# Optimization experiments

Hardware: AMD Instinct MI355X
Metric: run time of the kernel (lower is better)

## Reference

```python
import jax, jax.numpy as jnp
import numpy as np

N_HEAD = 8
HIDDEN = 512
EPS_LN = 1e-3  # keras LayerNormalization default epsilon


def layernorm(x, gamma, beta, eps=EPS_LN):
    mu = jnp.mean(x, axis=-1, keepdims=True)
    var = jnp.mean((x - mu) ** 2, axis=-1, keepdims=True)
    return (x - mu) * jax.lax.rsqrt(var + eps) * gamma + beta


def setup_inputs() -> dict:
    key = jax.random.key(0)
    ks = jax.random.split(key, 10)
    bs, NE, F = 512, 128, HIDDEN
    x = jax.random.normal(ks[0], (bs, NE, F), dtype=jnp.float32)
    mask = (jax.random.uniform(ks[1], (bs, 1, NE)) < 0.85).astype(jnp.float32)
    # guarantee at least one live entity per row
    mask = mask.at[:, :, 0].set(1.0)
    s = 1.0 / np.sqrt(F)
    Wqk = jax.random.normal(ks[2], (F, 2 * HIDDEN), dtype=jnp.float32) * s
    bqk = jnp.zeros((2 * HIDDEN,), jnp.float32)
    Wv = jax.random.normal(ks[3], (F, HIDDEN), dtype=jnp.float32) * s
    bv = jnp.zeros((HIDDEN,), jnp.float32)
    Wmlp = jax.random.normal(ks[4], (F, HIDDEN), dtype=jnp.float32) * s
    bmlp = jnp.zeros((HIDDEN,), jnp.float32)
    g_pre = jnp.ones((F,), jnp.float32)
    b_pre = jnp.zeros((F,), jnp.float32)
    g_post = jnp.ones((F,), jnp.float32)
    b_post = jnp.zeros((F,), jnp.float32)
    return dict(x=x, mask=mask, Wqk=Wqk, bqk=bqk, Wv=Wv, bv=bv,
                Wmlp=Wmlp, bmlp=bmlp, g_pre=g_pre, b_pre=b_pre,
                g_post=g_post, b_post=b_post)


def reference(x, mask, Wqk, bqk, Wv, bv, Wmlp, bmlp, g_pre, b_pre, g_post, b_post):
    bs, NE, F = x.shape
    h, d = N_HEAD, HIDDEN // N_HEAD
    x4 = x[:, None]  # (bs, 1, NE, F)

    # pre-norm only feeds qkv projections; residual uses raw x4
    inp = layernorm(x4, g_pre, b_pre)

    qk = (inp @ Wqk + bqk).reshape(bs, 1, NE, h, d, 2)
    q, k = qk[..., 0], qk[..., 1]                       # (bs,1,NE,h,d)
    v = (inp @ Wv + bv).reshape(bs, 1, NE, h, d)

    logits = jnp.einsum('btnhd,btmhd->bthnm', q, k) / np.sqrt(d)  # (bs,1,h,NE,NE)

    m5 = mask[:, :, None, None, :]                      # (bs,1,1,1,NE)
    logits = logits - (1.0 - m5) * 1e10
    logits = logits - jnp.max(logits, axis=-1, keepdims=True)
    un = jnp.exp(logits) * m5
    p = un / (jnp.sum(un, axis=-1, keepdims=True) + 1e-10)
    p = p * m5

    att = jnp.einsum('bthnm,btmhd->btnhd', p, v).reshape(bs, 1, NE, HIDDEN)
    a = att @ Wmlp + bmlp                               # mlp_layer=1, no activation
    y = x4 + a                                          # residual
    y = layernorm(y, g_post, b_post)

    # masked average pooling over entities
    mE = mask[..., None]                                # (bs,1,NE,1)
    pooled = jnp.sum(y * mE, axis=-2) / (jnp.sum(mE, axis=-2) + 1e-5)  # (bs,1,F)
    return pooled.reshape(bs, F)
```

## Files before the change

kernel.cpp:

```cpp
#include <hip/hip_runtime.h>
#include <hip/hip_bf16.h>


typedef __bf16 bf16;
typedef __bf16 bf16x8 __attribute__((ext_vector_type(8)));
typedef __bf16 bf16x4 __attribute__((ext_vector_type(4)));
typedef float f32x4 __attribute__((ext_vector_type(4)));
typedef unsigned u32x4 __attribute__((ext_vector_type(4)));

__device__ __forceinline__ f32x4 mfma16(bf16x8 a, bf16x8 b, f32x4 c) {
    return __builtin_amdgcn_mfma_f32_16x16x32_bf16(a, b, c, 0, 0, 0);
}

typedef const unsigned int __attribute__((address_space(1)))* gptr_t;
typedef unsigned int __attribute__((address_space(3)))* lptr_t;
__device__ __forceinline__ void gld16(const void* g, void* l) {
    __builtin_amdgcn_global_load_lds((gptr_t)g, (lptr_t)l, 16, 0, 0);
}

__device__ __forceinline__ unsigned pack2(float lo, float hi) {
    unsigned short a = __builtin_bit_cast(unsigned short, (bf16)lo);
    unsigned short b = __builtin_bit_cast(unsigned short, (bf16)hi);
    return (unsigned)a | ((unsigned)b << 16);
}

#define SWZ(byteoff, row) ((byteoff) ^ (((row) & 7) << 4))


__global__ __launch_bounds__(256) void prep_split_kernel(
    const float* __restrict__ Wqk, const float* __restrict__ bqk,
    const float* __restrict__ Wv, const float* __restrict__ bv,
    const float* __restrict__ Wmlp,
    bf16* __restrict__ Wqkv_s, bf16* __restrict__ Wmlp_t, float* __restrict__ bQKV)
{
    int t = blockIdx.x * 256 + threadIdx.x;
    if (t < 524288) {
        int k = t >> 10, c = t & 1023;
        int h = c >> 7, w7 = c & 127, d = w7 >> 1, isK = w7 & 1;
        int n = isK * 512 + h * 64 + d;
        int tn = n >> 7, nc = n & 127, kc = k >> 6, kw = k & 63;
        Wqkv_s[((size_t)(tn * 8 + kc) * 128 + nc) * 64 + kw] = (bf16)Wqk[t];
    } else if (t < 786432) {
        int u = t - 524288;
        int k = u >> 9, c = u & 511;
        int n = 1024 + c;
        int tn = n >> 7, nc = n & 127, kc = k >> 6, kw = k & 63;
        Wqkv_s[((size_t)(tn * 8 + kc) * 128 + nc) * 64 + kw] = (bf16)Wv[u];
    } else if (t < 1048576) {
        int u = t - 786432;
        int k = u >> 9, c = u & 511;
        int tn = c >> 7, nc = c & 127, kc = k >> 6, kw = k & 63;
        Wmlp_t[((size_t)(tn * 8 + kc) * 128 + nc) * 64 + kw] = (bf16)Wmlp[u];
    } else if (t < 1050112) {
        int j = t - 1048576;
        int region = j >> 9, w9 = j & 511, h = w9 >> 6, d = w9 & 63;
        float v;
        if (region == 0)      v = bqk[h * 128 + d * 2];
        else if (region == 1) v = bqk[h * 128 + d * 2 + 1];
        else                  v = bv[h * 64 + d];
        bQKV[j] = v;
    }
}

__global__ __launch_bounds__(256) void ln_kernel(
    const float* __restrict__ x, const float* __restrict__ g,
    const float* __restrict__ b, bf16* __restrict__ inp)
{
    int row = blockIdx.x * 4 + (threadIdx.x >> 6);
    int lane = threadIdx.x & 63;
    int k0 = lane * 8;
    const float* xr = x + (size_t)row * 512 + k0;
    f32x4 a0 = *(const f32x4*)xr;
    f32x4 a1 = *(const f32x4*)(xr + 4);
    float s = 0.f, ss = 0.f;
#pragma unroll
    for (int i = 0; i < 4; i++) {
        s += a0[i] + a1[i];
        ss += a0[i] * a0[i] + a1[i] * a1[i];
    }
#pragma unroll
    for (int m = 1; m < 64; m <<= 1) {
        s  += __shfl_xor(s, m, 64);
        ss += __shfl_xor(ss, m, 64);
    }
    float mu = s * (1.f / 512.f);
    float rstd = rsqrtf(ss * (1.f / 512.f) - mu * mu + 1e-3f);
    f32x4 g0 = *(const f32x4*)(g + k0);
    f32x4 g1 = *(const f32x4*)(g + k0 + 4);
    f32x4 b0 = *(const f32x4*)(b + k0);
    f32x4 b1 = *(const f32x4*)(b + k0 + 4);
    bf16x8 ov;
#pragma unroll
    for (int i = 0; i < 4; i++) {
        ov[i]     = (bf16)((a0[i] - mu) * rstd * g0[i] + b0[i]);
        ov[i + 4] = (bf16)((a1[i] - mu) * rstd * g1[i] + b1[i]);
    }
    *(bf16x8*)(inp + (size_t)row * 512 + k0) = ov;
}

__global__ __launch_bounds__(256) void qkv_gemm_kernel(
    const bf16* __restrict__ inp, const bf16* __restrict__ Wqkv_s,
    const float* __restrict__ bQKV,
    bf16* __restrict__ q, bf16* __restrict__ kbuf, bf16* __restrict__ vt)
{
    __shared__ __align__(16) bf16 As[128 * 64];
    __shared__ __align__(16) bf16 Bs[128 * 64];
    const int bid = blockIdx.x;
    const int idx = (bid & 7) * 768 + (bid >> 3);
    const int tm = idx / 12, tn = idx % 12;
    const int tid = threadIdx.x;
    const int w = tid >> 6, l = tid & 63;
    const int wr = w >> 1, wc = w & 1;
    const int l15 = l & 15, l4 = l >> 4;

    const f32x4 fz = {0.f, 0.f, 0.f, 0.f};
    f32x4 acc[4][4];
#pragma unroll
    for (int m = 0; m < 4; m++)
#pragma unroll
        for (int n = 0; n < 4; n++) acc[m][n] = fz;

    const int arow = l >> 3;
    const int axc = ((l & 7) ^ arow) * 8;
    const bf16* Abase = inp + (size_t)(tm * 128) * 512;
    const int rsw = (l15 & 7) << 4;

    for (int kc = 0; kc < 8; kc++) {
#pragma unroll
        for (int i = 0; i < 4; i++) {
            int rg = (i * 4 + w) * 8;
            gld16(Abase + (size_t)(rg + arow) * 512 + kc * 64 + axc,
                  As + (i * 4 + w) * 512);
        }
        const bf16* Bbase = Wqkv_s + (size_t)(tn * 8 + kc) * 8192;
#pragma unroll
        for (int i = 0; i < 4; i++) {
            gld16(Bbase + (size_t)((i * 4 + w) * 8 + arow) * 64 + axc,
                  Bs + (i * 4 + w) * 512);
        }
        __syncthreads();
#pragma unroll
        for (int kk = 0; kk < 2; kk++) {
            const int kb = (kk * 64 + l4 * 16) ^ rsw;
            bf16x8 af[4], bfr[4];
#pragma unroll
            for (int m = 0; m < 4; m++)
                af[m] = *(const bf16x8*)((const char*)As + (wr * 64 + m * 16 + l15) * 128 + kb);
#pragma unroll
            for (int n = 0; n < 4; n++)
                bfr[n] = *(const bf16x8*)((const char*)Bs + (wc * 64 + n * 16 + l15) * 128 + kb);
#pragma unroll
            for (int m = 0; m < 4; m++)
#pragma unroll
                for (int n = 0; n < 4; n++)
                    acc[m][n] = mfma16(af[m], bfr[n], acc[m][n]);
        }
        __syncthreads();
    }

    const int colBase = tn * 128 + wc * 64;
    const int mrowBase = tm * 128 + wr * 64;
#pragma unroll
    for (int n = 0; n < 4; n++) {
        int col = colBase + n * 16 + l15;
        float bias = bQKV[col];
        int within = col & 511, hh = within >> 6, dd = within & 63;
#pragma unroll
        for (int m = 0; m < 4; m++) {
            int mr0 = mrowBase + m * 16 + l4 * 4;
            int bb = mr0 >> 7, e0 = mr0 & 127;
            size_t base = (size_t)(bb * 8 + hh) * 8192;
            if (tn < 4) {
#pragma unroll
                for (int r = 0; r < 4; r++)
                    q[base + (size_t)(e0 + r) * 64 + dd] = (bf16)(acc[m][n][r] + bias);
            } else if (tn < 8) {
#pragma unroll
                for (int r = 0; r < 4; r++) {
                    int e = e0 + r;
                    kbuf[base + (size_t)e * 64 + (dd ^ ((e & 7) << 3))] = (bf16)(acc[m][n][r] + bias);
                }
            } else {
                bf16x4 pk;
#pragma unroll
                for (int r = 0; r < 4; r++) pk[r] = (bf16)(acc[m][n][r] + bias);
                *(bf16x4*)(vt + base + (size_t)dd * 128 + (e0 ^ ((dd & 7) << 3))) = pk;
            }
        }
    }
}

__global__ __launch_bounds__(512) void attn_fused_kernel(
    const bf16* __restrict__ q, const bf16* __restrict__ kbuf,
    const bf16* __restrict__ vt, const float* __restrict__ mask,
    bf16* __restrict__ att)
{
    __shared__ __align__(16) char Ks[2][128 * 128];
    __shared__ __align__(16) char VTs[2][64 * 256];
    __shared__ float mrow[128];

    const int b = blockIdx.x;
    const size_t bh0 = (size_t)b * 8;
    const int tid = threadIdx.x;
    const int w = tid >> 6, l = tid & 63;
    const int l15 = l & 15, l4 = l >> 4, R0 = w * 16;

    if (tid < 128) mrow[tid] = mask[b * 128 + tid];

    {
        const bf16* kb = kbuf + bh0 * 8192;
        const bf16* vb = vt + bh0 * 8192;
#pragma unroll
        for (int i = 0; i < 2; i++) {
            gld16(kb + ((i * 8 + w) * 64 + l) * 8, (bf16*)Ks[0] + (i * 8 + w) * 512);
            gld16(vb + ((i * 8 + w) * 64 + l) * 8, (bf16*)VTs[0] + (i * 8 + w) * 512);
        }
    }
    const bf16* qp0 = q + bh0 * 8192 + (size_t)(R0 + l15) * 64 + l4 * 8;
    bf16x8 afn0 = *(const bf16x8*)(qp0);
    bf16x8 afn1 = *(const bf16x8*)(qp0 + 32);
    __syncthreads();

    const f32x4 fz = {0.f, 0.f, 0.f, 0.f};
    for (int h = 0; h < 8; h++) {
        const int cur = h & 1;
        bf16x8 af0 = afn0, af1 = afn1;
        if (h < 7) {
            const bf16* kb = kbuf + (bh0 + h + 1) * 8192;
            const bf16* vb = vt + (bh0 + h + 1) * 8192;
#pragma unroll
            for (int i = 0; i < 2; i++) {
                gld16(kb + ((i * 8 + w) * 64 + l) * 8, (bf16*)Ks[cur ^ 1] + (i * 8 + w) * 512);
                gld16(vb + ((i * 8 + w) * 64 + l) * 8, (bf16*)VTs[cur ^ 1] + (i * 8 + w) * 512);
            }
            const bf16* qp = q + (bh0 + h + 1) * 8192 + (size_t)(R0 + l15) * 64 + l4 * 8;
            afn0 = *(const bf16x8*)(qp);
            afn1 = *(const bf16x8*)(qp + 32);
        }

        f32x4 accL[8];
#pragma unroll
        for (int n = 0; n < 8; n++) accL[n] = fz;
#pragma unroll
        for (int ks = 0; ks < 2; ks++) {
            bf16x8 bq = ks ? af1 : af0;
            const int k2 = ks * 64 + l4 * 16;
#pragma unroll
            for (int nt = 0; nt < 8; nt++) {
                const int krow = nt * 16 + l15;
                bf16x8 kf = *(const bf16x8*)(Ks[cur] + krow * 128 + (k2 ^ ((krow & 7) << 4)));
                accL[nt] = mfma16(kf, bq, accL[nt]);
            }
        }

        float mx = -1e30f;
#pragma unroll
        for (int nt = 0; nt < 8; nt++)
#pragma unroll
            for (int r = 0; r < 4; r++) {
                float mk = mrow[nt * 16 + l4 * 4 + r];
                float v = accL[nt][r] * 0.125f - (1.0f - mk) * 1e10f;
                accL[nt][r] = v;
                mx = fmaxf(mx, v);
            }
        mx = fmaxf(mx, __shfl_xor(mx, 16, 64));
        mx = fmaxf(mx, __shfl_xor(mx, 32, 64));
        float sum = 0.f;
#pragma unroll
        for (int nt = 0; nt < 8; nt++)
#pragma unroll
            for (int r = 0; r < 4; r++) {
                float mk = mrow[nt * 16 + l4 * 4 + r];
                float e = __expf(accL[nt][r] - mx) * mk;
                accL[nt][r] = e;
                sum += e;
            }
        sum += __shfl_xor(sum, 16, 64);
        sum += __shfl_xor(sum, 32, 64);
        const float inv = 1.0f / (sum + 1e-10f);

        unsigned pk[8][2];
#pragma unroll
        for (int nt = 0; nt < 8; nt++)
#pragma unroll
            for (int qq = 0; qq < 2; qq++)
                pk[nt][qq] = pack2(accL[nt][2 * qq] * inv, accL[nt][2 * qq + 1] * inv);

        f32x4 accO[4];
#pragma unroll
        for (int n = 0; n < 4; n++) accO[n] = fz;
        const int glo = l15 + ((l4 & 1) << 5);
#pragma unroll
        for (int ks = 0; ks < 4; ks++) {
            u32x4 pa4;
#pragma unroll
            for (int p = 0; p < 4; p++) {
                int srcl = glo + ((p >> 1) << 4);
                unsigned va = (unsigned)__shfl((int)pk[2 * ks][p & 1], srcl, 64);
                unsigned vb = (unsigned)__shfl((int)pk[2 * ks + 1][p & 1], srcl, 64);
                pa4[p] = (l4 & 2) ? vb : va;
            }
            bf16x8 pa = __builtin_bit_cast(bf16x8, pa4);
            const int e2 = ks * 64 + l4 * 16;
#pragma unroll
            for (int nt = 0; nt < 4; nt++) {
                const int d = nt * 16 + l15;
                bf16x8 vf = *(const bf16x8*)(VTs[cur] + d * 256 + (e2 ^ ((d & 7) << 4)));
                accO[nt] = mfma16(pa, vf, accO[nt]);
            }
        }

        bf16* outp = att + (size_t)(b * 128) * 512 + h * 64;
#pragma unroll
        for (int nt = 0; nt < 4; nt++) {
            const int d = nt * 16 + l15;
#pragma unroll
            for (int r = 0; r < 4; r++) {
                const int e = R0 + l4 * 4 + r;
                outp[(size_t)e * 512 + d] = (bf16)accO[nt][r];
            }
        }
        __syncthreads();
    }
}

__global__ __launch_bounds__(256) void mlp_gemm_kernel(
    const bf16* __restrict__ att, const bf16* __restrict__ Wmlp_t,
    const float* __restrict__ bmlp, float* __restrict__ y)
{
    __shared__ __align__(16) bf16 As[128 * 64];
    __shared__ __align__(16) bf16 Bs[128 * 64];
    const int bid = blockIdx.x;
    const int idx = (bid & 7) * 256 + (bid >> 3);
    const int tm = idx >> 2, tn = idx & 3;
    const int tid = threadIdx.x;
    const int w = tid >> 6, l = tid & 63;
    const int wr = w >> 1, wc = w & 1;
    const int l15 = l & 15, l4 = l >> 4;

    const f32x4 fz = {0.f, 0.f, 0.f, 0.f};
    f32x4 acc[4][4];
#pragma unroll
    for (int m = 0; m < 4; m++)
#pragma unroll
        for (int n = 0; n < 4; n++) acc[m][n] = fz;

    const int arow = l >> 3;
    const int axc = ((l & 7) ^ arow) * 8;
    const bf16* Abase = att + (size_t)(tm * 128) * 512;
    const int rsw = (l15 & 7) << 4;

    for (int kc = 0; kc < 8; kc++) {
#pragma unroll
        for (int i = 0; i < 4; i++) {
            int rg = (i * 4 + w) * 8;
            gld16(Abase + (size_t)(rg + arow) * 512 + kc * 64 + axc,
                  As + (i * 4 + w) * 512);
        }
        const bf16* Bbase = Wmlp_t + (size_t)(tn * 8 + kc) * 8192;
#pragma unroll
        for (int i = 0; i < 4; i++) {
            gld16(Bbase + (size_t)((i * 4 + w) * 8 + arow) * 64 + axc,
                  Bs + (i * 4 + w) * 512);
        }
        __syncthreads();
#pragma unroll
        for (int kk = 0; kk < 2; kk++) {
            const int kb = (kk * 64 + l4 * 16) ^ rsw;
            bf16x8 af[4], bfr[4];
#pragma unroll
            for (int m = 0; m < 4; m++)
                af[m] = *(const bf16x8*)((const char*)As + (wr * 64 + m * 16 + l15) * 128 + kb);
#pragma unroll
            for (int n = 0; n < 4; n++)
                bfr[n] = *(const bf16x8*)((const char*)Bs + (wc * 64 + n * 16 + l15) * 128 + kb);
#pragma unroll
            for (int m = 0; m < 4; m++)
#pragma unroll
                for (int n = 0; n < 4; n++)
                    acc[m][n] = mfma16(af[m], bfr[n], acc[m][n]);
        }
        __syncthreads();
    }

    const int colBase = tn * 128 + wc * 64;
    const int mrowBase = tm * 128 + wr * 64;
#pragma unroll
    for (int n = 0; n < 4; n++) {
        int col = colBase + n * 16 + l15;
        float bias = bmlp[col];
#pragma unroll
        for (int m = 0; m < 4; m++) {
            int row0 = mrowBase + m * 16 + l4 * 4;
#pragma unroll
            for (int r = 0; r < 4; r++)
                y[(size_t)(row0 + r) * 512 + col] = acc[m][n][r] + bias;
        }
    }
}

__global__ __launch_bounds__(512) void pool_kernel(
    const float* __restrict__ y, const float* __restrict__ x,
    const float* __restrict__ mask, const float* __restrict__ gpost,
    const float* __restrict__ bpost, float* __restrict__ out)
{
    __shared__ float partial[8][512];
    __shared__ float mrow[128];
    __shared__ float msum_s;

    const int b = blockIdx.x;
    const int tid = threadIdx.x;
    const int w = tid >> 6, l = tid & 63;
    const int k0 = l * 8;

    if (tid < 128) mrow[tid] = mask[b * 128 + tid];
    __syncthreads();
    if (w == 0) {
        float v = mrow[l] + mrow[64 + l];
#pragma unroll
        for (int m = 1; m < 64; m <<= 1) v += __shfl_xor(v, m, 64);
        if (l == 0) msum_s = v;
    }

    f32x4 g0 = *(const f32x4*)(gpost + k0);
    f32x4 g1 = *(const f32x4*)(gpost + k0 + 4);
    f32x4 b0 = *(const f32x4*)(bpost + k0);
    f32x4 b1 = *(const f32x4*)(bpost + k0 + 4);

    f32x4 a0 = {0.f, 0.f, 0.f, 0.f}, a1 = {0.f, 0.f, 0.f, 0.f};
    for (int i = 0; i < 16; i++) {
        int row = w * 16 + i;
        const float* yr = y + ((size_t)(b * 128 + row)) * 512 + k0;
        const float* xr = x + ((size_t)(b * 128 + row)) * 512 + k0;
        f32x4 v0 = *(const f32x4*)yr + *(const f32x4*)xr;
        f32x4 v1 = *(const f32x4*)(yr + 4) + *(const f32x4*)(xr + 4);
        float s = 0.f, ss = 0.f;
#pragma unroll
        for (int j = 0; j < 4; j++) {
            s += v0[j] + v1[j];
            ss += v0[j] * v0[j] + v1[j] * v1[j];
        }
#pragma unroll
        for (int m = 1; m < 64; m <<= 1) {
            s  += __shfl_xor(s, m, 64);
            ss += __shfl_xor(ss, m, 64);
        }
        float mu = s * (1.f / 512.f);
        float rstd = rsqrtf(ss * (1.f / 512.f) - mu * mu + 1e-3f);
        float mr = mrow[row];
#pragma unroll
        for (int j = 0; j < 4; j++) {
            a0[j] += ((v0[j] - mu) * rstd * g0[j] + b0[j]) * mr;
            a1[j] += ((v1[j] - mu) * rstd * g1[j] + b1[j]) * mr;
        }
    }
#pragma unroll
    for (int j = 0; j < 4; j++) {
        partial[w][k0 + j]     = a0[j];
        partial[w][k0 + 4 + j] = a1[j];
    }
    __syncthreads();
    float t = 0.f;
#pragma unroll
    for (int ww = 0; ww < 8; ww++) t += partial[ww][tid];
    out[(size_t)b * 512 + tid] = t / (msum_s + 1e-5f);
}

__global__ __launch_bounds__(256) void prep_kernel(
    const float* __restrict__ Wqk, const float* __restrict__ bqk,
    const float* __restrict__ Wv, const float* __restrict__ bv,
    const float* __restrict__ Wmlp,
    bf16* __restrict__ Wqkv_t, bf16* __restrict__ Wmlp_t, float* __restrict__ bQKV)
{
    int t = blockIdx.x * 256 + threadIdx.x;
    const int NQKV = 8 * 192 * 512;
    if (t < NQKV) {
        int h = t / (192 * 512);
        int rem = t - h * (192 * 512);
        int n = rem >> 9;
        int k = rem & 511;
        float v;
        if (n < 64)       v = Wqk[k * 1024 + h * 128 + n * 2];
        else if (n < 128) v = Wqk[k * 1024 + h * 128 + (n - 64) * 2 + 1];
        else              v = Wv[k * 512 + h * 64 + (n - 128)];
        Wqkv_t[t] = (bf16)v;
    } else {
        int u = t - NQKV;
        if (u < 512 * 512) {
            int col = u >> 9, k = u & 511;
            Wmlp_t[u] = (bf16)Wmlp[k * 512 + col];
        } else {
            int j = u - 512 * 512;
            if (j < 1536) {
                int h = j / 192, n = j - h * 192;
                float v;
                if (n < 64)       v = bqk[h * 128 + n * 2];
                else if (n < 128) v = bqk[h * 128 + (n - 64) * 2 + 1];
                else              v = bv[h * 64 + (n - 128)];
                bQKV[j] = v;
            }
        }
    }
}

__global__ __launch_bounds__(512) void attn_kernel(
    const bf16* __restrict__ inp, const float* __restrict__ mask,
    const bf16* __restrict__ Wqkv_t, const float* __restrict__ bQKV,
    bf16* __restrict__ att)
{
    __shared__ __align__(16) char Qs[128 * 128];
    __shared__ __align__(16) char Ks[128 * 128];
    __shared__ __align__(16) char VTs[64 * 256];
    __shared__ __align__(16) char Ps[128 * 256];
    __shared__ float mrow[128];

    const int bid = blockIdx.x;
    const int b = bid & 511;
    const int h = bid >> 9;
    const int tid = threadIdx.x;
    const int w = tid >> 6, l = tid & 63;
    const int l15 = l & 15, l4 = l >> 4;
    const int R0 = w * 16;

    if (tid < 128) mrow[tid] = mask[b * 128 + tid];

    const bf16* A  = inp + (size_t)(b * 128) * 512;
    const bf16* Wh = Wqkv_t + (size_t)h * 192 * 512;
    const f32x4 fz = {0.f, 0.f, 0.f, 0.f};

    f32x4 acc[12];
#pragma unroll
    for (int n = 0; n < 12; n++) acc[n] = fz;
    const bf16* aptr = A + (size_t)(R0 + l15) * 512 + l4 * 8;
#pragma unroll 4
    for (int ks = 0; ks < 16; ks++) {
        bf16x8 af = *(const bf16x8*)(aptr + ks * 32);
#pragma unroll
        for (int n = 0; n < 12; n++) {
            bf16x8 bfr = *(const bf16x8*)(Wh + (size_t)(n * 16 + l15) * 512 + ks * 32 + l4 * 8);
            acc[n] = mfma16(af, bfr, acc[n]);
        }
    }
#pragma unroll
    for (int n = 0; n < 12; n++) {
        int col = n * 16 + l15;
        float bias = bQKV[h * 192 + col];
#pragma unroll
        for (int r = 0; r < 4; r++) {
            int row = R0 + l4 * 4 + r;
            bf16 val = (bf16)(acc[n][r] + bias);
            if (n < 4) {
                *(bf16*)(Qs + row * 128 + SWZ(col * 2, row)) = val;
            } else if (n < 8) {
                *(bf16*)(Ks + row * 128 + SWZ((col - 64) * 2, row)) = val;
            } else {
                int d = col - 128;
                *(bf16*)(VTs + d * 256 + SWZ(row * 2, d)) = val;
            }
        }
    }
    __syncthreads();

    f32x4 accL[8];
#pragma unroll
    for (int n = 0; n < 8; n++) accL[n] = fz;
#pragma unroll
    for (int ks = 0; ks < 2; ks++) {
        int k = ks * 32 + l4 * 8;
        int qrow = R0 + l15;
        bf16x8 af = *(const bf16x8*)(Qs + qrow * 128 + SWZ(k * 2, qrow));
#pragma unroll
        for (int nt = 0; nt < 8; nt++) {
            int krow = nt * 16 + l15;
            bf16x8 bfr = *(const bf16x8*)(Ks + krow * 128 + SWZ(k * 2, krow));
            accL[nt] = mfma16(af, bfr, accL[nt]);
        }
    }
    float pv[32];
#pragma unroll
    for (int r = 0; r < 4; r++) {
        float mx = -1e30f;
#pragma unroll
        for (int nt = 0; nt < 8; nt++) {
            int colk = nt * 16 + l15;
            float v = accL[nt][r] * 0.125f - (1.0f - mrow[colk]) * 1e10f;
            pv[nt * 4 + r] = v;
            mx = fmaxf(mx, v);
        }
#pragma unroll
        for (int m = 1; m < 16; m <<= 1) mx = fmaxf(mx, __shfl_xor(mx, m, 64));
        float sum = 0.f;
#pragma unroll
        for (int nt = 0; nt < 8; nt++) {
            int colk = nt * 16 + l15;
            float e = __expf(pv[nt * 4 + r] - mx) * mrow[colk];
            pv[nt * 4 + r] = e;
            sum += e;
        }
#pragma unroll
        for (int m = 1; m < 16; m <<= 1) sum += __shfl_xor(sum, m, 64);
        float inv = 1.0f / (sum + 1e-10f);
        int prow = R0 + l4 * 4 + r;
#pragma unroll
        for (int nt = 0; nt < 8; nt++) {
            bf16 pb = (bf16)(pv[nt * 4 + r] * inv);
            *(bf16*)(Ps + prow * 256 + SWZ((nt * 16 + l15) * 2, prow)) = pb;
        }
    }
    __syncthreads();

    f32x4 accO[4];
#pragma unroll
    for (int n = 0; n < 4; n++) accO[n] = fz;
#pragma unroll
    for (int ks = 0; ks < 4; ks++) {
        int k = ks * 32 + l4 * 8;
        int prow = R0 + l15;
        bf16x8 af = *(const bf16x8*)(Ps + prow * 256 + SWZ(k * 2, prow));
#pragma unroll
        for (int nt = 0; nt < 4; nt++) {
            int d = nt * 16 + l15;
            bf16x8 bfr = *(const bf16x8*)(VTs + d * 256 + SWZ(k * 2, d));
            accO[nt] = mfma16(af, bfr, accO[nt]);
        }
    }
    bf16* outp = att + (size_t)(b * 128) * 512 + h * 64;
#pragma unroll
    for (int nt = 0; nt < 4; nt++) {
        int d = nt * 16 + l15;
#pragma unroll
        for (int r = 0; r < 4; r++) {
            int e = R0 + l4 * 4 + r;
            outp[(size_t)e * 512 + d] = (bf16)accO[nt][r];
        }
    }
}

__global__ __launch_bounds__(512) void mlp_kernel(
    const bf16* __restrict__ att, const bf16* __restrict__ Wmlp_t,
    const float* __restrict__ bmlp, const float* __restrict__ x,
    const float* __restrict__ mask, const float* __restrict__ gpost,
    const float* __restrict__ bpost, float* __restrict__ out)
{
    __shared__ float pool[512];
    __shared__ float gb[1024];
    __shared__ float mrow[128];
    __shared__ float msum_s;

    const int b = blockIdx.x;
    const int tid = threadIdx.x;
    const int w = tid >> 6, l = tid & 63;
    const int l15 = l & 15, l4 = l >> 4;
    const int R0 = w * 16;

    pool[tid] = 0.f;
    gb[tid] = gpost[tid];
    gb[512 + tid] = bpost[tid];
    if (tid < 128) mrow[tid] = mask[b * 128 + tid];
    __syncthreads();
    if (w == 0) {
        float v = mrow[l] + mrow[64 + l];
#pragma unroll
        for (int m = 1; m < 64; m <<= 1) v += __shfl_xor(v, m, 64);
        if (l == 0) msum_s = v;
    }

    const f32x4 fz = {0.f, 0.f, 0.f, 0.f};
    f32x4 acc[32];
#pragma unroll
    for (int n = 0; n < 32; n++) acc[n] = fz;
    const bf16* Ab = att + (size_t)(b * 128 + R0 + l15) * 512 + l4 * 8;
#pragma unroll 2
    for (int ks = 0; ks < 16; ks++) {
        bf16x8 af = *(const bf16x8*)(Ab + ks * 32);
#pragma unroll
        for (int nt = 0; nt < 32; nt++) {
            bf16x8 bfr = *(const bf16x8*)(Wmlp_t + (size_t)(nt * 16 + l15) * 512 + ks * 32 + l4 * 8);
            acc[nt] = mfma16(af, bfr, acc[nt]);
        }
    }
#pragma unroll
    for (int nt = 0; nt < 32; nt++) {
        int col = nt * 16 + l15;
        float bb = bmlp[col];
#pragma unroll
        for (int r = 0; r < 4; r++) {
            int row = R0 + l4 * 4 + r;
            acc[nt][r] = acc[nt][r] + bb + x[((size_t)b * 128 + row) * 512 + col];
        }
    }
    float mu[4], rs[4];
#pragma unroll
    for (int r = 0; r < 4; r++) {
        float s = 0.f, ss = 0.f;
#pragma unroll
        for (int nt = 0; nt < 32; nt++) {
            float v = acc[nt][r];
            s += v; ss += v * v;
        }
#pragma unroll
        for (int m = 1; m < 16; m <<= 1) {
            s  += __shfl_xor(s, m, 64);
            ss += __shfl_xor(ss, m, 64);
        }
        float m_ = s * (1.f / 512.f);
        mu[r] = m_;
        rs[r] = rsqrtf(ss * (1.f / 512.f) - m_ * m_ + 1e-3f);
    }
#pragma unroll
    for (int nt = 0; nt < 32; nt++) {
        int col = nt * 16 + l15;
        float g = gb[col], bb = gb[512 + col];
        float s = 0.f;
#pragma unroll
        for (int r = 0; r < 4; r++) {
            int row = R0 + l4 * 4 + r;
            float y = (acc[nt][r] - mu[r]) * rs[r] * g + bb;
            s += y * mrow[row];
        }
        atomicAdd(&pool[col], s);
    }
    __syncthreads();
    out[(size_t)b * 512 + tid] = pool[tid] / (msum_s + 1e-5f);
}

extern "C" void kernel_launch(void* const* d_in, const int* in_sizes, int n_in,
                              void* d_out, int out_size, void* d_ws, size_t ws_size,
                              hipStream_t stream)
{
    const float* x     = (const float*)d_in[0];
    const float* mask  = (const float*)d_in[1];
    const float* Wqk   = (const float*)d_in[2];
    const float* bqk   = (const float*)d_in[3];
    const float* Wv    = (const float*)d_in[4];
    const float* bv    = (const float*)d_in[5];
    const float* Wmlp  = (const float*)d_in[6];
    const float* bmlp  = (const float*)d_in[7];
    const float* gpre  = (const float*)d_in[8];
    const float* bpre  = (const float*)d_in[9];
    const float* gpost = (const float*)d_in[10];
    const float* bpost = (const float*)d_in[11];
    float* out = (float*)d_out;
    char* ws = (char*)d_ws;

    const size_t NEED_SPLIT = 270538752;
    if (ws_size >= NEED_SPLIT) {
        bf16*  q      = (bf16*)ws;
        bf16*  kbuf   = (bf16*)(ws + (size_t)67108864);
        bf16*  vt     = (bf16*)(ws + (size_t)134217728);
        bf16*  inp    = (bf16*)(ws + (size_t)201326592);
        bf16*  att    = inp;
        float* y      = (float*)ws;
        bf16*  Wqkv_s = (bf16*)(ws + (size_t)268435456);
        bf16*  Wmlp_t = (bf16*)(ws + (size_t)270008320);
        float* bQKV   = (float*)(ws + (size_t)270532608);

        prep_split_kernel<<<4103, 256, 0, stream>>>(Wqk, bqk, Wv, bv, Wmlp, Wqkv_s, Wmlp_t, bQKV);
        ln_kernel<<<16384, 256, 0, stream>>>(x, gpre, bpre, inp);
        qkv_gemm_kernel<<<6144, 256, 0, stream>>>(inp, Wqkv_s, bQKV, q, kbuf, vt);
        attn_fused_kernel<<<512, 512, 0, stream>>>(q, kbuf, vt, mask, att);
        mlp_gemm_kernel<<<2048, 256, 0, stream>>>(att, Wmlp_t, bmlp, y);
        pool_kernel<<<512, 512, 0, stream>>>(y, x, mask, gpost, bpost, out);
    } else {
        bf16*  inp    = (bf16*)ws;
        bf16*  att    = (bf16*)(ws + 67108864);
        bf16*  Wqkv_t = (bf16*)(ws + 134217728);
        bf16*  Wmlp_t = (bf16*)(ws + 134217728 + 1572864);
        float* bQKV   = (float*)(ws + 134217728 + 1572864 + 524288);

        prep_kernel<<<4103, 256, 0, stream>>>(Wqk, bqk, Wv, bv, Wmlp, Wqkv_t, Wmlp_t, bQKV);
        ln_kernel<<<16384, 256, 0, stream>>>(x, gpre, bpre, inp);
        attn_kernel<<<4096, 512, 0, stream>>>(inp, mask, Wqkv_t, bQKV, att);
        mlp_kernel<<<512, 512, 0, stream>>>(att, Wmlp_t, bmlp, x, mask, gpost, bpost, out);
    }
}
```

Measured before the change: 563.9 us.

## Double-buffer GEMM LDS tiles, store MLP output as bf16, coalesce weight prep writes

Both the QKV and MLP GEMMs now use two LDS buffers, so the next K-chunk is fetched while the current one is multiplied, hiding global load latency. The MLP output y is stored in bf16 instead of fp32, halving that intermediate's write and read traffic in the pool kernel at some precision cost. The weight-prep kernel is re-indexed so writes are contiguous and reads are gathered. Doubling shared memory per block may lower occupancy, and the loop appears to drop the barrier after the prefetch/compute step, which could cause a race on buffer reuse.

```diff
diff --git a/kernel.cpp b/kernel.cpp
--- a/kernel.cpp
+++ b/kernel.cpp
@@ -34,23 +34,26 @@
     bf16* __restrict__ Wqkv_s, bf16* __restrict__ Wmlp_t, float* __restrict__ bQKV)
 {
     int t = blockIdx.x * 256 + threadIdx.x;
-    if (t < 524288) {
-        int k = t >> 10, c = t & 1023;
-        int h = c >> 7, w7 = c & 127, d = w7 >> 1, isK = w7 & 1;
-        int n = isK * 512 + h * 64 + d;
-        int tn = n >> 7, nc = n & 127, kc = k >> 6, kw = k & 63;
-        Wqkv_s[((size_t)(tn * 8 + kc) * 128 + nc) * 64 + kw] = (bf16)Wqk[t];
-    } else if (t < 786432) {
-        int u = t - 524288;
-        int k = u >> 9, c = u & 511;
-        int n = 1024 + c;
-        int tn = n >> 7, nc = n & 127, kc = k >> 6, kw = k & 63;
-        Wqkv_s[((size_t)(tn * 8 + kc) * 128 + nc) * 64 + kw] = (bf16)Wv[u];
+    if (t < 786432) {
+        int tnkc = t >> 13;
+        int within = t & 8191;
+        int nc = within >> 6, kw = within & 63;
+        int tn = tnkc >> 3, kc = tnkc & 7;
+        int n = tn * 128 + nc, k = kc * 64 + kw;
+        float v;
+        if (n < 512)       v = Wqk[k * 1024 + (n >> 6) * 128 + (n & 63) * 2];
+        else if (n < 1024) { int nn = n - 512;
+                             v = Wqk[k * 1024 + (nn >> 6) * 128 + (nn & 63) * 2 + 1]; }
+        else               v = Wv[k * 512 + (n - 1024)];
+        Wqkv_s[t] = (bf16)v;
     } else if (t < 1048576) {
         int u = t - 786432;
-        int k = u >> 9, c = u & 511;
-        int tn = c >> 7, nc = c & 127, kc = k >> 6, kw = k & 63;
-        Wmlp_t[((size_t)(tn * 8 + kc) * 128 + nc) * 64 + kw] = (bf16)Wmlp[u];
+        int tnkc = u >> 13;
+        int within = u & 8191;
+        int nc = within >> 6, kw = within & 63;
+        int tn = tnkc >> 3, kc = tnkc & 7;
+        int n = tn * 128 + nc, k = kc * 64 + kw;
+        Wmlp_t[u] = (bf16)Wmlp[k * 512 + n];
     } else if (t < 1050112) {
         int j = t - 1048576;
         int region = j >> 9, w9 = j & 511, h = w9 >> 6, d = w9 & 63;
@@ -103,8 +106,8 @@
     const float* __restrict__ bQKV,
     bf16* __restrict__ q, bf16* __restrict__ kbuf, bf16* __restrict__ vt)
 {
-    __shared__ __align__(16) bf16 As[128 * 64];
-    __shared__ __align__(16) bf16 Bs[128 * 64];
+    __shared__ __align__(16) bf16 As[2][128 * 64];
+    __shared__ __align__(16) bf16 Bs[2][128 * 64];
     const int bid = blockIdx.x;
     const int idx = (bid & 7) * 768 + (bid >> 3);
     const int tm = idx / 12, tn = idx % 12;
@@ -123,32 +126,39 @@
     const int arow = l >> 3;
     const int axc = ((l & 7) ^ arow) * 8;
     const bf16* Abase = inp + (size_t)(tm * 128) * 512;
+    const bf16* Bbase0 = Wqkv_s + (size_t)tn * 8 * 8192;
     const int rsw = (l15 & 7) << 4;
 
+#pragma unroll
+    for (int i = 0; i < 4; i++) {
+        gld16(Abase + (size_t)((i * 4 + w) * 8 + arow) * 512 + axc,
+              As[0] + (i * 4 + w) * 512);
+        gld16(Bbase0 + (size_t)((i * 4 + w) * 8 + arow) * 64 + axc,
+              Bs[0] + (i * 4 + w) * 512);
+    }
+    __syncthreads();
+
     for (int kc = 0; kc < 8; kc++) {
-#pragma unroll
-        for (int i = 0; i < 4; i++) {
-            int rg = (i * 4 + w) * 8;
-            gld16(Abase + (size_t)(rg + arow) * 512 + kc * 64 + axc,
-                  As + (i * 4 + w) * 512);
-        }
-        const bf16* Bbase = Wqkv_s + (size_t)(tn * 8 + kc) * 8192;
-#pragma unroll
-        for (int i = 0; i < 4; i++) {
-            gld16(Bbase + (size_t)((i * 4 + w) * 8 + arow) * 64 + axc,
-                  Bs + (i * 4 + w) * 512);
-        }
-        __syncthreads();
+        const int cur = kc & 1;
+        if (kc < 7) {
+#pragma unroll
+            for (int i = 0; i < 4; i++) {
+                gld16(Abase + (size_t)((i * 4 + w) * 8 + arow) * 512 + (kc + 1) * 64 + axc,
+                      As[cur ^ 1] + (i * 4 + w) * 512);
+                gld16(Bbase0 + (size_t)(kc + 1) * 8192 + (size_t)((i * 4 + w) * 8 + arow) * 64 + axc,
+                      Bs[cur ^ 1] + (i * 4 + w) * 512);
+            }
+        }
 #pragma unroll
         for (int kk = 0; kk < 2; kk++) {
             const int kb = (kk * 64 + l4 * 16) ^ rsw;
             bf16x8 af[4], bfr[4];
 #pragma unroll
             for (int m = 0; m < 4; m++)
-                af[m] = *(const bf16x8*)((const char*)As + (wr * 64 + m * 16 + l15) * 128 + kb);
+                af[m] = *(const bf16x8*)((const char*)As[cur] + (wr * 64 + m * 16 + l15) * 128 + kb);
 #pragma unroll
             for (int n = 0; n < 4; n++)
-                bfr[n] = *(const bf16x8*)((const char*)Bs + (wc * 64 + n * 16 + l15) * 128 + kb);
+                bfr[n] = *(const bf16x8*)((const char*)Bs[cur] + (wc * 64 + n * 16 + l15) * 128 + kb);
 #pragma unroll
             for (int m = 0; m < 4; m++)
 #pragma unroll
@@ -326,10 +336,10 @@
 
 __global__ __launch_bounds__(256) void mlp_gemm_kernel(
     const bf16* __restrict__ att, const bf16* __restrict__ Wmlp_t,
-    const float* __restrict__ bmlp, float* __restrict__ y)
-{
-    __shared__ __align__(16) bf16 As[128 * 64];
-    __shared__ __align__(16) bf16 Bs[128 * 64];
+    const float* __restrict__ bmlp, bf16* __restrict__ y)
+{
+    __shared__ __align__(16) bf16 As[2][128 * 64];
+    __shared__ __align__(16) bf16 Bs[2][128 * 64];
     const int bid = blockIdx.x;
     const int idx = (bid & 7) * 256 + (bid >> 3);
     const int tm = idx >> 2, tn = idx & 3;
@@ -348,32 +358,39 @@
     const int arow = l >> 3;
     const int axc = ((l & 7) ^ arow) * 8;
     const bf16* Abase = att + (size_t)(tm * 128) * 512;
+    const bf16* Bbase0 = Wmlp_t + (size_t)tn * 8 * 8192;
     const int rsw = (l15 & 7) << 4;
 
+#pragma unroll
+    for (int i = 0; i < 4; i++) {
+        gld16(Abase + (size_t)((i * 4 + w) * 8 + arow) * 512 + axc,
+              As[0] + (i * 4 + w) * 512);
+        gld16(Bbase0 + (size_t)((i * 4 + w) * 8 + arow) * 64 + axc,
+              Bs[0] + (i * 4 + w) * 512);
+    }
+    __syncthreads();
+
     for (int kc = 0; kc < 8; kc++) {
-#pragma unroll
-        for (int i = 0; i < 4; i++) {
-            int rg = (i * 4 + w) * 8;
-            gld16(Abase + (size_t)(rg + arow) * 512 + kc * 64 + axc,
-                  As + (i * 4 + w) * 512);
-        }
-        const bf16* Bbase = Wmlp_t + (size_t)(tn * 8 + kc) * 8192;
-#pragma unroll
-        for (int i = 0; i < 4; i++) {
-            gld16(Bbase + (size_t)((i * 4 + w) * 8 + arow) * 64 + axc,
-                  Bs + (i * 4 + w) * 512);
-        }
-        __syncthreads();
+        const int cur = kc & 1;
+        if (kc < 7) {
+#pragma unroll
+            for (int i = 0; i < 4; i++) {
+                gld16(Abase + (size_t)((i * 4 + w) * 8 + arow) * 512 + (kc + 1) * 64 + axc,
+                      As[cur ^ 1] + (i * 4 + w) * 512);
+                gld16(Bbase0 + (size_t)(kc + 1) * 8192 + (size_t)((i * 4 + w) * 8 + arow) * 64 + axc,
+                      Bs[cur ^ 1] + (i * 4 + w) * 512);
+            }
+        }
 #pragma unroll
         for (int kk = 0; kk < 2; kk++) {
             const int kb = (kk * 64 + l4 * 16) ^ rsw;
             bf16x8 af[4], bfr[4];
 #pragma unroll
             for (int m = 0; m < 4; m++)
-                af[m] = *(const bf16x8*)((const char*)As + (wr * 64 + m * 16 + l15) * 128 + kb);
+                af[m] = *(const bf16x8*)((const char*)As[cur] + (wr * 64 + m * 16 + l15) * 128 + kb);
 #pragma unroll
             for (int n = 0; n < 4; n++)
-                bfr[n] = *(const bf16x8*)((const char*)Bs + (wc * 64 + n * 16 + l15) * 128 + kb);
+                bfr[n] = *(const bf16x8*)((const char*)Bs[cur] + (wc * 64 + n * 16 + l15) * 128 + kb);
 #pragma unroll
             for (int m = 0; m < 4; m++)
 #pragma unroll
@@ -394,13 +411,13 @@
             int row0 = mrowBase + m * 16 + l4 * 4;
 #pragma unroll
             for (int r = 0; r < 4; r++)
-                y[(size_t)(row0 + r) * 512 + col] = acc[m][n][r] + bias;
+                y[(size_t)(row0 + r) * 512 + col] = (bf16)(acc[m][n][r] + bias);
         }
     }
 }
 
 __global__ __launch_bounds__(512) void pool_kernel(
-    const float* __restrict__ y, const float* __restrict__ x,
+    const bf16* __restrict__ y, const float* __restrict__ x,
     const float* __restrict__ mask, const float* __restrict__ gpost,
     const float* __restrict__ bpost, float* __restrict__ out)
 {
@@ -430,10 +447,15 @@
     f32x4 a0 = {0.f, 0.f, 0.f, 0.f}, a1 = {0.f, 0.f, 0.f, 0.f};
     for (int i = 0; i < 16; i++) {
         int row = w * 16 + i;
-        const float* yr = y + ((size_t)(b * 128 + row)) * 512 + k0;
+        const bf16*  yr = y + ((size_t)(b * 128 + row)) * 512 + k0;
         const float* xr = x + ((size_t)(b * 128 + row)) * 512 + k0;
-        f32x4 v0 = *(const f32x4*)yr + *(const f32x4*)xr;
-        f32x4 v1 = *(const f32x4*)(yr + 4) + *(const f32x4*)(xr + 4);
+        bf16x8 yv = *(const bf16x8*)yr;
+        f32x4 v0, v1;
+#pragma unroll
+        for (int j = 0; j < 4; j++) {
+            v0[j] = (float)yv[j]     + xr[j];
+            v1[j] = (float)yv[j + 4] + xr[j + 4];
+        }
         float s = 0.f, ss = 0.f;
 #pragma unroll
         for (int j = 0; j < 4; j++) {
@@ -750,7 +772,7 @@
         bf16*  vt     = (bf16*)(ws + (size_t)134217728);
         bf16*  inp    = (bf16*)(ws + (size_t)201326592);
         bf16*  att    = inp;
-        float* y      = (float*)ws;
+        bf16*  y      = (bf16*)ws;
         bf16*  Wqkv_s = (bf16*)(ws + (size_t)268435456);
         bf16*  Wmlp_t = (bf16*)(ws + (size_t)270008320);
         float* bQKV   = (float*)(ws + (size_t)270532608);
```

Measured after the change: 532.7 us. 1.06x faster.
